# Kernel optimization log

Hardware: AMD Instinct MI355X
Metric: run time of the kernel (lower is better)

Reference implementation:

```python
import jax, jax.numpy as jnp
import numpy as np

N = 100000
E = 1600000
IN_C = 128
OUT_C = 64


def setup_inputs() -> dict:
    key = jax.random.key(0)
    ks = jax.random.split(key, 8)
    x = jax.random.normal(ks[0], (N, IN_C), dtype=jnp.float32)
    edge_index = jax.random.randint(ks[1], (2, E), 0, N, dtype=jnp.int64)
    neg_edge_index = jax.random.randint(ks[2], (2, E), 0, N, dtype=jnp.int64)
    # GCNConv params (glorot-ish init)
    W = jax.random.normal(ks[3], (IN_C, OUT_C), dtype=jnp.float32) / np.sqrt(IN_C)
    b = jnp.zeros((OUT_C,), dtype=jnp.float32)
    # classifier Linear(2*out_channels, 2)
    Wc = jax.random.normal(ks[4], (2 * OUT_C, 2), dtype=jnp.float32) / np.sqrt(2 * OUT_C)
    bc = jnp.zeros((2,), dtype=jnp.float32)
    return {"x": x, "edge_index": edge_index, "neg_edge_index": neg_edge_index,
            "W": W, "b": b, "Wc": Wc, "bc": bc}


def gcn_conv(x, edge_index, W, b):
    # Add self-loops, symmetric normalization: D^{-1/2} (A+I) D^{-1/2} X W + b
    loops = jnp.arange(N, dtype=edge_index.dtype)
    src = jnp.concatenate([edge_index[0], loops])  # [E+N]
    dst = jnp.concatenate([edge_index[1], loops])  # [E+N]
    deg = jax.ops.segment_sum(jnp.ones_like(dst, dtype=x.dtype), dst, num_segments=N)
    dinv = jax.lax.rsqrt(jnp.maximum(deg, 1e-12))
    norm = dinv[src] * dinv[dst]                   # [E+N]
    xw = x @ W                                     # [N, OUT_C] transform first (cheaper)
    msg = norm[:, None] * xw[src]                  # gather + scale
    out = jax.ops.segment_sum(msg, dst, num_segments=N)  # scatter-add aggregate
    return out + b


def reference(x, edge_index, neg_edge_index, W, b, Wc, bc):
    h = jax.nn.relu(gcn_conv(x, edge_index, W, b))           # [N, OUT_C]
    total = jnp.concatenate([edge_index, neg_edge_index], axis=1)  # [2, 2E]
    edge_feat = jnp.concatenate([h[total[0]], h[total[1]]], axis=1)  # [2E, 2*OUT_C]
    return edge_feat @ Wc + bc                               # [2E, 2]
```

## Files before the change

kernel.cpp:

```cpp
#include <hip/hip_runtime.h>

#define N_NODES 100000
#define N_EDGES 1600000
#define IN_C    128
#define OUT_C   64

#define SB_NODES 512
#define NSB  ((N_NODES + SB_NODES - 1) / SB_NODES)
#define SCAP 9216
#define ACHUNK 4096
#define NABLK ((N_EDGES + ACHUNK - 1) / ACHUNK)

__device__ inline unsigned pack_bf16x2(float lo, float hi) {
    unsigned a = __float_as_uint(lo), b2 = __float_as_uint(hi);
    a  += 0x7fff + ((a  >> 16) & 1);
    b2 += 0x7fff + ((b2 >> 16) & 1);
    return (a >> 16) | (b2 & 0xffff0000u);
}
__device__ inline float bf_lo(unsigned v) { return __uint_as_float(v << 16); }
__device__ inline float bf_hi(unsigned v) { return __uint_as_float(v & 0xffff0000u); }

__global__ void zero_kernel(int* __restrict__ cursor) {
    int i = blockIdx.x * blockDim.x + threadIdx.x;
    if (i < NSB) cursor[i] = 0;
}

__global__ __launch_bounds__(256) void sorta_kernel(const int* __restrict__ ei,
                                                    int* __restrict__ cursor,
                                                    int* __restrict__ sb) {
    __shared__ int histW[4][NSB];
    __shared__ int base_[NSB];
    __shared__ int cur[NSB];
    const int t = threadIdx.x, w = t >> 6;
    const long long e0 = (long long)blockIdx.x * ACHUNK;
    for (int i = t; i < 4 * NSB; i += 256) (&histW[0][0])[i] = 0;
    __syncthreads();
    const int* dsts = ei + N_EDGES;
#pragma unroll
    for (int k = 0; k < ACHUNK / 1024; ++k) {
        long long i4 = e0 / 4 + t + k * 256;
        if (i4 * 4 + 3 < N_EDGES) {
            int4 d = *(const int4*)&dsts[i4 * 4];
            atomicAdd(&histW[w][d.x >> 9], 1);
            atomicAdd(&histW[w][d.y >> 9], 1);
            atomicAdd(&histW[w][d.z >> 9], 1);
            atomicAdd(&histW[w][d.w >> 9], 1);
        }
    }
    __syncthreads();
    if (t < NSB) {
        int c = histW[0][t] + histW[1][t] + histW[2][t] + histW[3][t];
        base_[t] = c ? atomicAdd(&cursor[t], c) : 0;
        cur[t] = 0;
    }
    __syncthreads();
#pragma unroll
    for (int k = 0; k < ACHUNK / 1024; ++k) {
        long long i4 = e0 / 4 + t + k * 256;
        if (i4 * 4 + 3 < N_EDGES) {
            int4 s4 = *(const int4*)&ei[i4 * 4];
            int4 d4 = *(const int4*)&dsts[i4 * 4];
            int sv[4] = {s4.x, s4.y, s4.z, s4.w};
            int dv[4] = {d4.x, d4.y, d4.z, d4.w};
#pragma unroll
            for (int j = 0; j < 4; ++j) {
                int bk = dv[j] >> 9;
                int pos = base_[bk] + atomicAdd(&cur[bk], 1);
                if (pos < SCAP)
                    sb[bk * SCAP + pos] = sv[j] * SB_NODES + (dv[j] & (SB_NODES - 1));
            }
        }
    }
}

__global__ __launch_bounds__(256) void sortb_kernel(const int* __restrict__ cursor,
                                                    int* __restrict__ sb,
                                                    float* __restrict__ dinv,
                                                    int* __restrict__ rowbeg,
                                                    int* __restrict__ rowend) {
    __shared__ int hist[SB_NODES];
    __shared__ int pref[SB_NODES + 1];
    __shared__ int cur[SB_NODES];
    __shared__ int sc[256];
    __shared__ int sorted[SCAP];
    const int t = threadIdx.x, b = blockIdx.x;
    for (int k = t; k < SB_NODES; k += 256) { hist[k] = 0; cur[k] = 0; }
    __syncthreads();
    int m = cursor[b]; if (m > SCAP) m = SCAP;
    int* bb = sb + b * SCAP;
    for (int i = t; i < m; i += 256) atomicAdd(&hist[bb[i] & (SB_NODES - 1)], 1);
    __syncthreads();
    int c0 = hist[2 * t], c1 = hist[2 * t + 1];
    int tsum = c0 + c1;
    sc[t] = tsum;
    __syncthreads();
    for (int off = 1; off < 256; off <<= 1) {
        int u = (t >= off) ? sc[t - off] : 0;
        __syncthreads();
        sc[t] += u;
        __syncthreads();
    }
    int excl = sc[t] - tsum;
    pref[2 * t]     = excl;
    pref[2 * t + 1] = excl + c0;
    if (t == 255) pref[SB_NODES] = sc[255];
    __syncthreads();
    for (int i = t; i < m; i += 256) {
        int e = bb[i];
        int dl = e & (SB_NODES - 1);
        int pos = pref[dl] + atomicAdd(&cur[dl], 1);
        sorted[pos] = e >> 9;
    }
    __syncthreads();
    for (int i = t; i < m; i += 256) bb[i] = sorted[i];
    for (int k = t; k < SB_NODES; k += 256) {
        int n = b * SB_NODES + k;
        if (n < N_NODES) {
            rowbeg[n] = b * SCAP + pref[k];
            rowend[n] = b * SCAP + pref[k + 1];
            dinv[n]   = rsqrtf((float)hist[k] + 1.0f);
        }
    }
}

#define XN  32
#define SXS 132
__global__ __launch_bounds__(256) void xws_kernel(const float* __restrict__ x,
                                                  const float* __restrict__ W,
                                                  const float* __restrict__ dinv,
                                                  unsigned* __restrict__ xwsh) {
    __shared__ float sW[IN_C * OUT_C];
    __shared__ float sx[XN * SXS];
    const int t = threadIdx.x;
    const int n0 = blockIdx.x * XN;
    const float4* W4 = (const float4*)W;
    float4* sW4 = (float4*)sW;
#pragma unroll
    for (int k = 0; k < 8; ++k) sW4[t + k * 256] = W4[t + k * 256];
#pragma unroll
    for (int k = 0; k < 4; ++k) {
        int idx = (t + k * 256) * 4;
        int r = idx >> 7, kk = idx & 127;
        int n = n0 + r;
        float4 v = (n < N_NODES) ? *(const float4*)&x[(long long)n * IN_C + kk]
                                 : make_float4(0.f, 0.f, 0.f, 0.f);
        *(float4*)&sx[r * SXS + kk] = v;
    }
    __syncthreads();
    const int r  = t >> 4;
    const int cq = (t & 15) << 2;
    float4 a0 = make_float4(0.f,0.f,0.f,0.f), a1 = a0;
#pragma unroll 8
    for (int k = 0; k < IN_C; ++k) {
        float x0 = sx[r * SXS + k];
        float x1 = sx[(r + 16) * SXS + k];
        float4 wv = *(const float4*)&sW[(k << 6) + cq];
        a0.x = fmaf(x0, wv.x, a0.x); a0.y = fmaf(x0, wv.y, a0.y);
        a0.z = fmaf(x0, wv.z, a0.z); a0.w = fmaf(x0, wv.w, a0.w);
        a1.x = fmaf(x1, wv.x, a1.x); a1.y = fmaf(x1, wv.y, a1.y);
        a1.z = fmaf(x1, wv.z, a1.z); a1.w = fmaf(x1, wv.w, a1.w);
    }
    int na = n0 + r, nb = n0 + r + 16;
    if (na < N_NODES) {
        float di = dinv[na];
        uint2 o = make_uint2(pack_bf16x2(a0.x * di, a0.y * di),
                             pack_bf16x2(a0.z * di, a0.w * di));
        *(uint2*)&xwsh[(long long)na * 32 + ((t & 15) << 1)] = o;
    }
    if (nb < N_NODES) {
        float di = dinv[nb];
        uint2 o = make_uint2(pack_bf16x2(a1.x * di, a1.y * di),
                             pack_bf16x2(a1.z * di, a1.w * di));
        *(uint2*)&xwsh[(long long)nb * 32 + ((t & 15) << 1)] = o;
    }
}

__global__ __launch_bounds__(256) void aggnode_kernel(
    const int* __restrict__ rowbeg, const int* __restrict__ rowend,
    const int* __restrict__ srcs, const float* __restrict__ dinv,
    const unsigned* __restrict__ xwsh, const float* __restrict__ b,
    const float* __restrict__ Wc, const float* __restrict__ bc,
    float2* __restrict__ p, float2* __restrict__ q) {
    const int lane = threadIdx.x & 63;
    int node = __builtin_amdgcn_readfirstlane(blockIdx.x * 4 + (threadIdx.x >> 6));
    const int beg = rowbeg[node], end = rowend[node];
    const int half = lane >> 5, hl = lane & 31;
    float ax0 = 0.f, ay0 = 0.f, ax1 = 0.f, ay1 = 0.f;
    float ax2 = 0.f, ay2 = 0.f, ax3 = 0.f, ay3 = 0.f;
    int i = beg;
    for (; i + 7 < end; i += 8) {
        int s0 = srcs[i + 0], s1 = srcs[i + 1], s2 = srcs[i + 2], s3 = srcs[i + 3];
        int s4 = srcs[i + 4], s5 = srcs[i + 5], s6 = srcs[i + 6], s7 = srcs[i + 7];
        unsigned v0 = xwsh[(half ? s1 : s0) * 32 + hl];
        unsigned v1 = xwsh[(half ? s3 : s2) * 32 + hl];
        unsigned v2 = xwsh[(half ? s5 : s4) * 32 + hl];
        unsigned v3 = xwsh[(half ? s7 : s6) * 32 + hl];
        ax0 += bf_lo(v0); ay0 += bf_hi(v0);
        ax1 += bf_lo(v1); ay1 += bf_hi(v1);
        ax2 += bf_lo(v2); ay2 += bf_hi(v2);
        ax3 += bf_lo(v3); ay3 += bf_hi(v3);
    }
    for (; i + 1 < end; i += 2) {
        int sa = srcs[i], sb2 = srcs[i + 1];
        unsigned v = xwsh[(half ? sb2 : sa) * 32 + hl];
        ax0 += bf_lo(v); ay0 += bf_hi(v);
    }
    if (i < end) {
        int s = srcs[i];
        unsigned v = xwsh[s * 32 + hl];
        if (!half) { ax1 += bf_lo(v); ay1 += bf_hi(v); }
    }
    float ax = (ax0 + ax1) + (ax2 + ax3);
    float ay = (ay0 + ay1) + (ay2 + ay3);
    ax += __shfl(ax, hl + 32);
    ay += __shfl(ay, hl + 32);
    unsigned vs = xwsh[node * 32 + hl];
    ax += bf_lo(vs); ay += bf_hi(vs);
    float di = dinv[node];
    float2 b2 = ((const float2*)b)[hl];
    float h0 = fmaxf(fmaf(di, ax, b2.x), 0.f);
    float h1 = fmaxf(fmaf(di, ay, b2.y), 0.f);
    float4 wcs = ((const float4*)Wc)[hl];
    float4 wcd = ((const float4*)(Wc + 2 * OUT_C))[hl];
    float p0 = h0 * wcs.x + h1 * wcs.z;
    float p1 = h0 * wcs.y + h1 * wcs.w;
    float q0 = h0 * wcd.x + h1 * wcd.z;
    float q1 = h0 * wcd.y + h1 * wcd.w;
#pragma unroll
    for (int off = 16; off; off >>= 1) {
        p0 += __shfl_down(p0, off); p1 += __shfl_down(p1, off);
        q0 += __shfl_down(q0, off); q1 += __shfl_down(q1, off);
    }
    if (lane == 0) {
        p[node] = make_float2(p0 + bc[0], p1 + bc[1]);
        q[node] = make_float2(q0, q1);
    }
}

__global__ void edge_kernel(const int* __restrict__ ei, const int* __restrict__ nei,
                            const float2* __restrict__ p, const float2* __restrict__ q,
                            float4* __restrict__ out4) {
    int idx = blockIdx.x * blockDim.x + threadIdx.x;
    if (idx >= 2 * N_EDGES / 4) return;
    int e4 = idx * 4;
    const int *S, *D;
    int off;
    if (e4 < N_EDGES) { S = ei;  D = ei  + N_EDGES; off = e4; }
    else              { S = nei; D = nei + N_EDGES; off = e4 - N_EDGES; }
    int4 s4 = *(const int4*)&S[off];
    int4 d4 = *(const int4*)&D[off];
    float2 pa = p[s4.x], qa = q[d4.x];
    float2 pb = p[s4.y], qb = q[d4.y];
    float2 pc = p[s4.z], qc = q[d4.z];
    float2 pd = p[s4.w], qd = q[d4.w];
    out4[idx * 2]     = make_float4(pa.x + qa.x, pa.y + qa.y, pb.x + qb.x, pb.y + qb.y);
    out4[idx * 2 + 1] = make_float4(pc.x + qc.x, pc.y + qc.y, pd.x + qd.x, pd.y + qd.y);
}

extern "C" void kernel_launch(void* const* d_in, const int* in_sizes, int n_in,
                              void* d_out, int out_size, void* d_ws, size_t ws_size,
                              hipStream_t stream) {
    const float* x   = (const float*)d_in[0];
    const int*   ei  = (const int*)  d_in[1];
    const int*   nei = (const int*)  d_in[2];
    const float* W   = (const float*)d_in[3];
    const float* b   = (const float*)d_in[4];
    const float* Wc  = (const float*)d_in[5];
    const float* bc  = (const float*)d_in[6];

    int*      wsI    = (int*)d_ws;
    float*    dinv   = (float*)wsI;
    unsigned* xwsh   = (unsigned*)(wsI + 100352);
    float*    p      = (float*)(wsI + 3300352);
    float*    q      = (float*)(wsI + 3501056);
    int*      cursor = wsI + 3701760;
    int*      rowbeg = wsI + 3702016;
    int*      rowend = wsI + 3802368;
    int*      sbuf   = wsI + 3902720;

    const int B = 256;
    zero_kernel<<<1, B, 0, stream>>>(cursor);
    sorta_kernel<<<NABLK, B, 0, stream>>>(ei, cursor, sbuf);
    sortb_kernel<<<NSB, B, 0, stream>>>(cursor, sbuf, dinv, rowbeg, rowend);
    xws_kernel<<<(N_NODES + XN - 1) / XN, B, 0, stream>>>(x, W, dinv, xwsh);
    aggnode_kernel<<<N_NODES / 4, B, 0, stream>>>(rowbeg, rowend, sbuf, dinv, xwsh,
                                                  b, Wc, bc, (float2*)p, (float2*)q);
    edge_kernel<<<(2 * N_EDGES / 4 + B - 1) / B, B, 0, stream>>>(
        ei, nei, (const float2*)p, (const float2*)q, (float4*)d_out);
}
```

Before: 254.7 us.

## Replace per-node CSR sort with bucket-level shared-memory atomic aggregation

Removes the second sort pass that built per-node CSR rows. Edges are bucketed by destination into 256-node buckets, and each block accumulates its bucket's messages into a shared-memory fp32 accumulator with LDS atomics. Degrees are now counted with global atomics in the first sort pass, and dinv is recomputed on the fly. This trades a kernel launch and a sort for heavy LDS atomic contention, 64 KB of LDS per block, and only 391 aggregation blocks, which may underfill the GPU.

```diff
diff --git a/kernel.cpp b/kernel.cpp
--- a/kernel.cpp
+++ b/kernel.cpp
@@ -5,9 +5,9 @@
 #define IN_C    128
 #define OUT_C   64
 
-#define SB_NODES 512
-#define NSB  ((N_NODES + SB_NODES - 1) / SB_NODES)
-#define SCAP 9216
+#define SBN   256
+#define NSB   ((N_NODES + SBN - 1) / SBN)
+#define SCAP  4608
 #define ACHUNK 4096
 #define NABLK ((N_EDGES + ACHUNK - 1) / ACHUNK)
 
@@ -20,12 +20,14 @@
 __device__ inline float bf_lo(unsigned v) { return __uint_as_float(v << 16); }
 __device__ inline float bf_hi(unsigned v) { return __uint_as_float(v & 0xffff0000u); }
 
-__global__ void zero_kernel(int* __restrict__ cursor) {
+__global__ void zero_kernel(int* __restrict__ deg, int* __restrict__ cursor) {
     int i = blockIdx.x * blockDim.x + threadIdx.x;
-    if (i < NSB) cursor[i] = 0;
+    if (i < N_NODES) deg[i] = 0;
+    if (i < NSB)     cursor[i] = 0;
 }
 
 __global__ __launch_bounds__(256) void sorta_kernel(const int* __restrict__ ei,
+                                                    int* __restrict__ deg,
                                                     int* __restrict__ cursor,
                                                     int* __restrict__ sb) {
     __shared__ int histW[4][NSB];
@@ -41,17 +43,21 @@
         long long i4 = e0 / 4 + t + k * 256;
         if (i4 * 4 + 3 < N_EDGES) {
             int4 d = *(const int4*)&dsts[i4 * 4];
-            atomicAdd(&histW[w][d.x >> 9], 1);
-            atomicAdd(&histW[w][d.y >> 9], 1);
-            atomicAdd(&histW[w][d.z >> 9], 1);
-            atomicAdd(&histW[w][d.w >> 9], 1);
-        }
-    }
-    __syncthreads();
-    if (t < NSB) {
-        int c = histW[0][t] + histW[1][t] + histW[2][t] + histW[3][t];
-        base_[t] = c ? atomicAdd(&cursor[t], c) : 0;
-        cur[t] = 0;
+            atomicAdd(&histW[w][d.x >> 8], 1);
+            atomicAdd(&histW[w][d.y >> 8], 1);
+            atomicAdd(&histW[w][d.z >> 8], 1);
+            atomicAdd(&histW[w][d.w >> 8], 1);
+            atomicAdd(&deg[d.x], 1);
+            atomicAdd(&deg[d.y], 1);
+            atomicAdd(&deg[d.z], 1);
+            atomicAdd(&deg[d.w], 1);
+        }
+    }
+    __syncthreads();
+    for (int i = t; i < NSB; i += 256) {
+        int c = histW[0][i] + histW[1][i] + histW[2][i] + histW[3][i];
+        base_[i] = c ? atomicAdd(&cursor[i], c) : 0;
+        cur[i] = 0;
     }
     __syncthreads();
 #pragma unroll
@@ -64,61 +70,11 @@
             int dv[4] = {d4.x, d4.y, d4.z, d4.w};
 #pragma unroll
             for (int j = 0; j < 4; ++j) {
-                int bk = dv[j] >> 9;
+                int bk = dv[j] >> 8;
                 int pos = base_[bk] + atomicAdd(&cur[bk], 1);
                 if (pos < SCAP)
-                    sb[bk * SCAP + pos] = sv[j] * SB_NODES + (dv[j] & (SB_NODES - 1));
+                    sb[bk * SCAP + pos] = (sv[j] << 8) | (dv[j] & (SBN - 1));
             }
-        }
-    }
-}
-
-__global__ __launch_bounds__(256) void sortb_kernel(const int* __restrict__ cursor,
-                                                    int* __restrict__ sb,
-                                                    float* __restrict__ dinv,
-                                                    int* __restrict__ rowbeg,
-                                                    int* __restrict__ rowend) {
-    __shared__ int hist[SB_NODES];
-    __shared__ int pref[SB_NODES + 1];
-    __shared__ int cur[SB_NODES];
-    __shared__ int sc[256];
-    __shared__ int sorted[SCAP];
-    const int t = threadIdx.x, b = blockIdx.x;
-    for (int k = t; k < SB_NODES; k += 256) { hist[k] = 0; cur[k] = 0; }
-    __syncthreads();
-    int m = cursor[b]; if (m > SCAP) m = SCAP;
-    int* bb = sb + b * SCAP;
-    for (int i = t; i < m; i += 256) atomicAdd(&hist[bb[i] & (SB_NODES - 1)], 1);
-    __syncthreads();
-    int c0 = hist[2 * t], c1 = hist[2 * t + 1];
-    int tsum = c0 + c1;
-    sc[t] = tsum;
-    __syncthreads();
-    for (int off = 1; off < 256; off <<= 1) {
-        int u = (t >= off) ? sc[t - off] : 0;
-        __syncthreads();
-        sc[t] += u;
-        __syncthreads();
-    }
-    int excl = sc[t] - tsum;
-    pref[2 * t]     = excl;
-    pref[2 * t + 1] = excl + c0;
-    if (t == 255) pref[SB_NODES] = sc[255];
-    __syncthreads();
-    for (int i = t; i < m; i += 256) {
-        int e = bb[i];
-        int dl = e & (SB_NODES - 1);
-        int pos = pref[dl] + atomicAdd(&cur[dl], 1);
-        sorted[pos] = e >> 9;
-    }
-    __syncthreads();
-    for (int i = t; i < m; i += 256) bb[i] = sorted[i];
-    for (int k = t; k < SB_NODES; k += 256) {
-        int n = b * SB_NODES + k;
-        if (n < N_NODES) {
-            rowbeg[n] = b * SCAP + pref[k];
-            rowend[n] = b * SCAP + pref[k + 1];
-            dinv[n]   = rsqrtf((float)hist[k] + 1.0f);
         }
     }
 }
@@ -127,7 +83,7 @@
 #define SXS 132
 __global__ __launch_bounds__(256) void xws_kernel(const float* __restrict__ x,
                                                   const float* __restrict__ W,
-                                                  const float* __restrict__ dinv,
+                                                  const int* __restrict__ deg,
                                                   unsigned* __restrict__ xwsh) {
     __shared__ float sW[IN_C * OUT_C];
     __shared__ float sx[XN * SXS];
@@ -162,78 +118,81 @@
     }
     int na = n0 + r, nb = n0 + r + 16;
     if (na < N_NODES) {
-        float di = dinv[na];
+        float di = rsqrtf((float)deg[na] + 1.0f);
         uint2 o = make_uint2(pack_bf16x2(a0.x * di, a0.y * di),
                              pack_bf16x2(a0.z * di, a0.w * di));
         *(uint2*)&xwsh[(long long)na * 32 + ((t & 15) << 1)] = o;
     }
     if (nb < N_NODES) {
-        float di = dinv[nb];
+        float di = rsqrtf((float)deg[nb] + 1.0f);
         uint2 o = make_uint2(pack_bf16x2(a1.x * di, a1.y * di),
                              pack_bf16x2(a1.z * di, a1.w * di));
         *(uint2*)&xwsh[(long long)nb * 32 + ((t & 15) << 1)] = o;
     }
 }
 
-__global__ __launch_bounds__(256) void aggnode_kernel(
-    const int* __restrict__ rowbeg, const int* __restrict__ rowend,
-    const int* __restrict__ srcs, const float* __restrict__ dinv,
-    const unsigned* __restrict__ xwsh, const float* __restrict__ b,
-    const float* __restrict__ Wc, const float* __restrict__ bc,
+__global__ __launch_bounds__(256) void aggbucket_kernel(
+    const int* __restrict__ cursor, const int* __restrict__ sb,
+    const int* __restrict__ deg, const unsigned* __restrict__ xwsh,
+    const float* __restrict__ b, const float* __restrict__ Wc,
+    const float* __restrict__ bc,
     float2* __restrict__ p, float2* __restrict__ q) {
-    const int lane = threadIdx.x & 63;
-    int node = __builtin_amdgcn_readfirstlane(blockIdx.x * 4 + (threadIdx.x >> 6));
-    const int beg = rowbeg[node], end = rowend[node];
-    const int half = lane >> 5, hl = lane & 31;
-    float ax0 = 0.f, ay0 = 0.f, ax1 = 0.f, ay1 = 0.f;
-    float ax2 = 0.f, ay2 = 0.f, ax3 = 0.f, ay3 = 0.f;
-    int i = beg;
-    for (; i + 7 < end; i += 8) {
-        int s0 = srcs[i + 0], s1 = srcs[i + 1], s2 = srcs[i + 2], s3 = srcs[i + 3];
-        int s4 = srcs[i + 4], s5 = srcs[i + 5], s6 = srcs[i + 6], s7 = srcs[i + 7];
-        unsigned v0 = xwsh[(half ? s1 : s0) * 32 + hl];
-        unsigned v1 = xwsh[(half ? s3 : s2) * 32 + hl];
-        unsigned v2 = xwsh[(half ? s5 : s4) * 32 + hl];
-        unsigned v3 = xwsh[(half ? s7 : s6) * 32 + hl];
-        ax0 += bf_lo(v0); ay0 += bf_hi(v0);
-        ax1 += bf_lo(v1); ay1 += bf_hi(v1);
-        ax2 += bf_lo(v2); ay2 += bf_hi(v2);
-        ax3 += bf_lo(v3); ay3 += bf_hi(v3);
-    }
-    for (; i + 1 < end; i += 2) {
-        int sa = srcs[i], sb2 = srcs[i + 1];
-        unsigned v = xwsh[(half ? sb2 : sa) * 32 + hl];
-        ax0 += bf_lo(v); ay0 += bf_hi(v);
-    }
-    if (i < end) {
-        int s = srcs[i];
-        unsigned v = xwsh[s * 32 + hl];
-        if (!half) { ax1 += bf_lo(v); ay1 += bf_hi(v); }
-    }
-    float ax = (ax0 + ax1) + (ax2 + ax3);
-    float ay = (ay0 + ay1) + (ay2 + ay3);
-    ax += __shfl(ax, hl + 32);
-    ay += __shfl(ay, hl + 32);
-    unsigned vs = xwsh[node * 32 + hl];
-    ax += bf_lo(vs); ay += bf_hi(vs);
-    float di = dinv[node];
-    float2 b2 = ((const float2*)b)[hl];
-    float h0 = fmaxf(fmaf(di, ax, b2.x), 0.f);
-    float h1 = fmaxf(fmaf(di, ay, b2.y), 0.f);
-    float4 wcs = ((const float4*)Wc)[hl];
-    float4 wcd = ((const float4*)(Wc + 2 * OUT_C))[hl];
-    float p0 = h0 * wcs.x + h1 * wcs.z;
-    float p1 = h0 * wcs.y + h1 * wcs.w;
-    float q0 = h0 * wcd.x + h1 * wcd.z;
-    float q1 = h0 * wcd.y + h1 * wcd.w;
-#pragma unroll
-    for (int off = 16; off; off >>= 1) {
-        p0 += __shfl_down(p0, off); p1 += __shfl_down(p1, off);
-        q0 += __shfl_down(q0, off); q1 += __shfl_down(q1, off);
-    }
-    if (lane == 0) {
-        p[node] = make_float2(p0 + bc[0], p1 + bc[1]);
-        q[node] = make_float2(q0, q1);
+    __shared__ float acc[SBN * OUT_C];
+    const int t = threadIdx.x, bkt = blockIdx.x;
+    float4* a4 = (float4*)acc;
+#pragma unroll
+    for (int k = 0; k < 16; ++k) a4[t + k * 256] = make_float4(0.f, 0.f, 0.f, 0.f);
+    __syncthreads();
+    int m = cursor[bkt]; if (m > SCAP) m = SCAP;
+    const int* bb = sb + bkt * SCAP;
+    const int hw = t >> 5;
+    const int hl = t & 31;
+    int i = hw;
+    for (; i + 8 < m; i += 16) {
+        int ea = bb[i], eb = bb[i + 8];
+        unsigned va = xwsh[((unsigned)(ea >> 8) << 5) + hl];
+        unsigned vb = xwsh[((unsigned)(eb >> 8) << 5) + hl];
+        int da = (ea & (SBN - 1)) << 6, db = (eb & (SBN - 1)) << 6;
+        atomicAdd(&acc[da + 2 * hl],     bf_lo(va));
+        atomicAdd(&acc[da + 2 * hl + 1], bf_hi(va));
+        atomicAdd(&acc[db + 2 * hl],     bf_lo(vb));
+        atomicAdd(&acc[db + 2 * hl + 1], bf_hi(vb));
+    }
+    if (i < m) {
+        int ea = bb[i];
+        unsigned va = xwsh[((unsigned)(ea >> 8) << 5) + hl];
+        int da = (ea & (SBN - 1)) << 6;
+        atomicAdd(&acc[da + 2 * hl],     bf_lo(va));
+        atomicAdd(&acc[da + 2 * hl + 1], bf_hi(va));
+    }
+    __syncthreads();
+    for (int it = 0; it < 32; ++it) {
+        int dl = (hw << 5) + it;
+        int node = (bkt << 8) + dl;
+        if (node >= N_NODES) break;
+        float ax = acc[(dl << 6) + 2 * hl];
+        float ay = acc[(dl << 6) + 2 * hl + 1];
+        unsigned vs = xwsh[((unsigned)node << 5) + hl];
+        ax += bf_lo(vs); ay += bf_hi(vs);
+        float di = rsqrtf((float)deg[node] + 1.0f);
+        float2 b2 = ((const float2*)b)[hl];
+        float h0 = fmaxf(fmaf(di, ax, b2.x), 0.f);
+        float h1 = fmaxf(fmaf(di, ay, b2.y), 0.f);
+        float4 wcs = ((const float4*)Wc)[hl];
+        float4 wcd = ((const float4*)(Wc + 2 * OUT_C))[hl];
+        float p0 = h0 * wcs.x + h1 * wcs.z;
+        float p1 = h0 * wcs.y + h1 * wcs.w;
+        float q0 = h0 * wcd.x + h1 * wcd.z;
+        float q1 = h0 * wcd.y + h1 * wcd.w;
+#pragma unroll
+        for (int off = 16; off; off >>= 1) {
+            p0 += __shfl_down(p0, off, 32); p1 += __shfl_down(p1, off, 32);
+            q0 += __shfl_down(q0, off, 32); q1 += __shfl_down(q1, off, 32);
+        }
+        if (hl == 0) {
+            p[node] = make_float2(p0 + bc[0], p1 + bc[1]);
+            q[node] = make_float2(q0, q1);
+        }
     }
 }
 
@@ -269,22 +228,19 @@
     const float* bc  = (const float*)d_in[6];
 
     int*      wsI    = (int*)d_ws;
-    float*    dinv   = (float*)wsI;
+    int*      deg    = wsI;
     unsigned* xwsh   = (unsigned*)(wsI + 100352);
     float*    p      = (float*)(wsI + 3300352);
     float*    q      = (float*)(wsI + 3501056);
     int*      cursor = wsI + 3701760;
-    int*      rowbeg = wsI + 3702016;
-    int*      rowend = wsI + 3802368;
-    int*      sbuf   = wsI + 3902720;
+    int*      sbuf   = wsI + 3702208;
 
     const int B = 256;
-    zero_kernel<<<1, B, 0, stream>>>(cursor);
-    sorta_kernel<<<NABLK, B, 0, stream>>>(ei, cursor, sbuf);
-    sortb_kernel<<<NSB, B, 0, stream>>>(cursor, sbuf, dinv, rowbeg, rowend);
-    xws_kernel<<<(N_NODES + XN - 1) / XN, B, 0, stream>>>(x, W, dinv, xwsh);
-    aggnode_kernel<<<N_NODES / 4, B, 0, stream>>>(rowbeg, rowend, sbuf, dinv, xwsh,
-                                                  b, Wc, bc, (float2*)p, (float2*)q);
+    zero_kernel<<<(N_NODES + B - 1) / B, B, 0, stream>>>(deg, cursor);
+    sorta_kernel<<<NABLK, B, 0, stream>>>(ei, deg, cursor, sbuf);
+    xws_kernel<<<(N_NODES + XN - 1) / XN, B, 0, stream>>>(x, W, deg, xwsh);
+    aggbucket_kernel<<<NSB, B, 0, stream>>>(cursor, sbuf, deg, xwsh,
+                                            b, Wc, bc, (float2*)p, (float2*)q);
     edge_kernel<<<(2 * N_EDGES / 4 + B - 1) / B, B, 0, stream>>>(
         ei, nei, (const float2*)p, (const float2*)q, (float4*)d_out);
 }
```

Result: slower. 953.8 us (+274.5%).
